# Kernel tuning notes

Hardware: AMD Instinct MI355X
Metric: run time of the kernel (lower is better)

The kernel has to match this reference:

```python
import jax, jax.numpy as jnp
import numpy as np

DN = ('NCHW', 'OIHW', 'NCHW')


def conv2d(x, w, b, stride):
    y = jax.lax.conv_general_dilated(x, w, (stride, stride), 'VALID', dimension_numbers=DN)
    return y + b[None, :, None, None]


def split_heads(t, heads):
    # 'B (c h) H W -> B h (H W) c'  (channel index = c*heads + h)
    B, C, H, W = t.shape
    c = C // heads
    t = t.reshape(B, c, heads, H * W)
    return jnp.transpose(t, (0, 2, 3, 1))  # [B, h, HW, c]


def setup_inputs() -> dict:
    key = jax.random.key(0)
    ks = jax.random.split(key, 7)
    B, dim, H, W = 4, 256, 128, 128
    inner, p = 256, 8
    s = 0.02
    return {
        'x':  jax.random.normal(ks[0], (B, dim, H, W), jnp.float32),
        'Wq': jax.random.normal(ks[1], (inner, dim, 1, 1), jnp.float32) * s,
        'bq': jax.random.normal(ks[2], (inner,), jnp.float32) * s,
        'Wk': jax.random.normal(ks[3], (inner, dim, p, p), jnp.float32) * s,
        'bk': jax.random.normal(ks[4], (inner,), jnp.float32) * s,
        'Wv': jax.random.normal(ks[5], (inner, dim, p, p), jnp.float32) * s,
        'bv': jax.random.normal(ks[6], (inner,), jnp.float32) * s,
    }


def reference(x, Wq, bq, Wk, bk, Wv, bv):
    heads = 8
    p = Wk.shape[-1]
    B, C, H, W = x.shape
    q = conv2d(x, Wq, bq, 1)      # [B, inner, H, W]
    k = conv2d(x, Wk, bk, p)      # [B, inner, H/p, W/p]
    v = conv2d(x, Wv, bv, p)
    q = split_heads(q, heads)     # [B, h, HW, c]
    k = split_heads(k, heads)     # [B, h, K, c]
    v = split_heads(v, heads)
    # NOTE: original module applies no 1/sqrt(d) scaling
    dots = jnp.einsum('bhnc,bhkc->bhnk', q, k)
    attn = jax.nn.softmax(dots, axis=-1)
    out = jnp.einsum('bhnk,bhkc->bhnc', attn, v)  # [B, h, HW, c]
    # 'B h (H W) c -> B (c h) H W'
    c = out.shape[-1]
    out = jnp.transpose(out, (0, 3, 1, 2)).reshape(B, c * heads, H, W)
    return out
```

## Files before the change

### kernel.cpp

```cpp
#include <hip/hip_runtime.h>
#include <stdint.h>

typedef short sh4 __attribute__((ext_vector_type(4)));
typedef short short8 __attribute__((ext_vector_type(8)));
typedef float f32x4 __attribute__((ext_vector_type(4)));
typedef _Float16 half4 __attribute__((ext_vector_type(4)));
typedef _Float16 half8 __attribute__((ext_vector_type(8)));
typedef unsigned int uint2v __attribute__((ext_vector_type(2)));

__device__ __forceinline__ short f2h(float f) {
    _Float16 h = (_Float16)f;
    return __builtin_bit_cast(short, h);
}

__device__ __forceinline__ f32x4 mfma_k32(short8 a, short8 b, f32x4 c) {
    return __builtin_amdgcn_mfma_f32_16x16x32_f16(
        __builtin_bit_cast(half8, a), __builtin_bit_cast(half8, b), c, 0, 0, 0);
}
__device__ __forceinline__ f32x4 mfma_k16(half4 a, half4 b, f32x4 c) {
    return __builtin_amdgcn_mfma_f32_16x16x16f16(a, b, c, 0, 0, 0);
}
__device__ __forceinline__ unsigned int pkrtz(float a, float b) {
    return __builtin_bit_cast(unsigned int, __builtin_amdgcn_cvt_pkrtz(a, b));
}


__device__ __forceinline__ void transpose64(const float* __restrict__ src,
                                            short* __restrict__ dst,
                                            int srcSlowStride, int dstRowStride) {
    __shared__ float tile[64][65];
    const int t = threadIdx.x;
#pragma unroll
    for (int i = 0; i < 16; ++i) {
        int idx = i * 256 + t;
        int fast = idx & 63, slow = idx >> 6;
        tile[slow][fast] = src[(long)slow * srcSlowStride + fast];
    }
    __syncthreads();
#pragma unroll
    for (int i = 0; i < 2; ++i) {
        int ch = i * 256 + t;
        int fast = ch >> 3, sg = ch & 7;
        short8 v;
#pragma unroll
        for (int j = 0; j < 8; ++j) v[j] = f2h(tile[sg * 8 + j][fast]);
        *(short8*)(dst + (long)fast * dstRowStride + sg * 8) = v;
    }
}

__global__ __launch_bounds__(256) void k_pack_x(const float* __restrict__ x,
                                                short* __restrict__ xn) {
    int bi = blockIdx.x;
    int ct = bi & 3, pxt = (bi >> 2) & 255, b = bi >> 10;
    const float* src = x + (((long)(b * 256 + ct * 64)) << 14) + (long)pxt * 64;
    short* dst = xn + (((long)(b << 14) + pxt * 64) * 256) + ct * 64;
    transpose64(src, dst, 16384, 256);
}

__global__ __launch_bounds__(256) void k_pack_w(const float* __restrict__ wk,
                                                const float* __restrict__ wv,
                                                short* __restrict__ wp) {
    int bi = blockIdx.x;
    int ct = bi & 3, oc = bi >> 2;
    const float* base = (oc < 256) ? (wk + (long)oc * 16384) : (wv + (long)(oc - 256) * 16384);
    const float* src = base + ct * 4096;
    short* dst = wp + (long)oc * 16384 + ct * 64;
    transpose64(src, dst, 64, 256);
}

__global__ __launch_bounds__(256) void k_pack_wq(const float* __restrict__ wq,
                                                 short* __restrict__ wqp) {
    int i = blockIdx.x * 256 + threadIdx.x;
    wqp[i] = f2h(wq[i]);
}

__global__ __launch_bounds__(256) void k_kv_gemm(const short* __restrict__ xn,
                                                 const short* __restrict__ wp,
                                                 float* __restrict__ part) {
    __shared__ short Al[128 * 64];
    __shared__ short Bl[64 * 64];
    int bid = blockIdx.x;
    int wg = (bid & 7) * 64 + (bid >> 3);
    int nb = wg & 7, pm = (wg >> 3) & 7, kc = wg >> 6;
    int t = threadIdx.x, l = t & 63, w = t >> 6;
    int wm = w >> 1, wn = w & 1;
    int low = l & 15, q = l >> 4;

    f32x4 acc[4][2];
#pragma unroll
    for (int mt = 0; mt < 4; ++mt)
#pragma unroll
        for (int nt = 0; nt < 2; ++nt) acc[mt][nt] = (f32x4){0.f, 0.f, 0.f, 0.f};

    for (int kk = 0; kk < 32; ++kk) {
        short8 va[4], vb[2];
#pragma unroll
        for (int i = 0; i < 4; ++i) {
            int g = i * 256 + t;
            int row = g >> 3, lg = g & 7;
            int patch = pm * 128 + row;
            int kg = kc * 2048 + kk * 64 + lg * 8;
            int dydx = kg >> 8, cc = kg & 255;
            int bb = patch >> 8, pid = patch & 255;
            int ph = pid >> 4, pw = pid & 15;
            int px = (ph * 8 + (dydx >> 3)) * 128 + pw * 8 + (dydx & 7);
            va[i] = *(const short8*)(xn + ((long)(bb << 14) + px) * 256 + cc);
        }
#pragma unroll
        for (int i = 0; i < 2; ++i) {
            int g = i * 256 + t;
            int row = g >> 3, lg = g & 7;
            int oc = nb * 64 + row;
            int kg = kc * 2048 + kk * 64 + lg * 8;
            vb[i] = *(const short8*)(wp + (long)oc * 16384 + kg);
        }
#pragma unroll
        for (int i = 0; i < 4; ++i) {
            int g = i * 256 + t;
            int row = g >> 3, lg = g & 7;
            *(short8*)(Al + row * 64 + ((lg ^ (row & 7)) * 8)) = va[i];
        }
#pragma unroll
        for (int i = 0; i < 2; ++i) {
            int g = i * 256 + t;
            int row = g >> 3, lg = g & 7;
            *(short8*)(Bl + row * 64 + ((lg ^ (row & 7)) * 8)) = vb[i];
        }
        __syncthreads();
#pragma unroll
        for (int ks = 0; ks < 2; ++ks) {
            short8 af[4], bf[2];
#pragma unroll
            for (int mt = 0; mt < 4; ++mt) {
                int row = wm * 64 + mt * 16 + low;
                int lg = ks * 4 + q;
                af[mt] = *(const short8*)(Al + row * 64 + ((lg ^ (row & 7)) * 8));
            }
#pragma unroll
            for (int nt = 0; nt < 2; ++nt) {
                int row = wn * 32 + nt * 16 + low;
                int lg = ks * 4 + q;
                bf[nt] = *(const short8*)(Bl + row * 64 + ((lg ^ (row & 7)) * 8));
            }
#pragma unroll
            for (int mt = 0; mt < 4; ++mt)
#pragma unroll
                for (int nt = 0; nt < 2; ++nt)
                    acc[mt][nt] = mfma_k32(af[mt], bf[nt], acc[mt][nt]);
        }
        __syncthreads();
    }
#pragma unroll
    for (int mt = 0; mt < 4; ++mt) {
        int patch = pm * 128 + wm * 64 + mt * 16 + q * 4;
#pragma unroll
        for (int nt = 0; nt < 2; ++nt) {
            int oc = nb * 64 + wn * 32 + nt * 16 + low;
#pragma unroll
            for (int r = 0; r < 4; ++r)
                part[((long)kc * 1024 + patch + r) * 512 + oc] = acc[mt][nt][r];
        }
    }
}

__global__ __launch_bounds__(256) void k_kv_fin(const float* __restrict__ part,
                                                const float* __restrict__ bk,
                                                const float* __restrict__ bv,
                                                short* __restrict__ kp,
                                                short* __restrict__ vp) {
    int idx = blockIdx.x * 256 + threadIdx.x;
    int oc = idx & 511, patch = idx >> 9;
    float s = 0.f;
#pragma unroll
    for (int kc = 0; kc < 8; ++kc) s += part[(long)kc * 524288 + idx];
    int b = patch >> 8, key = patch & 255;
    if (oc < 256) {
        s += bk[oc];
        kp[(((long)(b * 8 + (oc & 7)) * 256) + key) * 32 + (oc >> 3)] = f2h(s);
    } else {
        int o = oc - 256;
        s += bv[o];
        vp[(((long)(b * 8 + (o & 7)) * 32) + (o >> 3)) * 256 + key] = f2h(s);
    }
}

__global__ __launch_bounds__(256) void k_q_gemm(const short* __restrict__ xn,
                                                const short* __restrict__ wqp,
                                                const float* __restrict__ bq,
                                                short* __restrict__ qp) {
    __shared__ short Tb[64 * 256];
    int bi = blockIdx.x;
    int b = bi >> 8, tile = bi & 255;
    long px0 = (long)tile * 64;
    int t = threadIdx.x, l = t & 63, w = t >> 6;
    int low = l & 15, q = l >> 4;

    const short* xb = xn + (((long)(b << 14)) + px0) * 256;

    float bqv[4];
#pragma unroll
    for (int nt = 0; nt < 4; ++nt) bqv[nt] = bq[w * 64 + nt * 16 + low];

    f32x4 acc[4][4];
#pragma unroll
    for (int mt = 0; mt < 4; ++mt)
#pragma unroll
        for (int nt = 0; nt < 4; ++nt) acc[mt][nt] = (f32x4){0.f, 0.f, 0.f, 0.f};

#pragma unroll
    for (int kstep = 0; kstep < 8; ++kstep) {
        short8 af[4], bf[4];
#pragma unroll
        for (int mt = 0; mt < 4; ++mt)
            af[mt] = *(const short8*)(xb + (mt * 16 + low) * 256 + kstep * 32 + q * 8);
#pragma unroll
        for (int nt = 0; nt < 4; ++nt)
            bf[nt] = *(const short8*)(wqp + (w * 64 + nt * 16 + low) * 256 + kstep * 32 + q * 8);
#pragma unroll
        for (int mt = 0; mt < 4; ++mt)
#pragma unroll
            for (int nt = 0; nt < 4; ++nt)
                acc[mt][nt] = mfma_k32(af[mt], bf[nt], acc[mt][nt]);
    }
#pragma unroll
    for (int mt = 0; mt < 4; ++mt)
#pragma unroll
        for (int nt = 0; nt < 4; ++nt) {
            int oc = w * 64 + nt * 16 + low;
            int h8 = oc & 7, cc = oc >> 3;
            int gi = h8 * 4 + (cc >> 3);
#pragma unroll
            for (int r = 0; r < 4; ++r) {
                int px = mt * 16 + q * 4 + r;
                Tb[px * 256 + ((gi ^ (px & 7)) * 8) + (cc & 7)] =
                    f2h(acc[mt][nt][r] + bqv[nt]);
            }
        }
    __syncthreads();
#pragma unroll
    for (int i = 0; i < 8; ++i) {
        int g = i * 256 + t;
        int pxl = g >> 5, g16 = g & 31;
        int hh = g16 >> 2, oct = g16 & 3;
        short8 v = *(const short8*)(Tb + pxl * 256 + ((g16 ^ (pxl & 7)) * 8));
        *(short8*)(qp + (((long)(b * 8 + hh) * 16384) + px0 + pxl) * 32 + oct * 8) = v;
    }
}

__global__ __launch_bounds__(256) void k_attn(const short* __restrict__ qp,
                                              const short* __restrict__ kp,
                                              const short* __restrict__ vp,
                                              float* __restrict__ out) {
    __shared__ short Kl[256 * 32];
    __shared__ short Vl[32 * 264];
    int bi = blockIdx.x;
    int tile = bi & 127, h = (bi >> 7) & 7, b = bi >> 10;
    int bh = b * 8 + h;
    long px0 = (long)tile * 128;
    int t = threadIdx.x, l = t & 63, w = t >> 6;
    int low = l & 15, q = l >> 4;

    const short* kbase = kp + (long)bh * 8192;
    const short* vbase = vp + (long)bh * 8192;
    const short* qbase = qp + (long)bh * 16384 * 32;

#pragma unroll
    for (int i = 0; i < 4; ++i) {
        int g = i * 256 + t;
        *(short8*)(Kl + g * 8) = *(const short8*)(kbase + g * 8);
    }
#pragma unroll
    for (int i = 0; i < 4; ++i) {
        int g = i * 256 + t;
        int c = g >> 5, k8 = g & 31;
        *(short8*)(Vl + c * 264 + k8 * 8) = *(const short8*)(vbase + c * 256 + k8 * 8);
    }
    short8 bq2[2];
#pragma unroll
    for (int nt = 0; nt < 2; ++nt) {
        long px = px0 + w * 32 + nt * 16 + low;
        bq2[nt] = *(const short8*)(qbase + px * 32 + q * 8);
    }
    __syncthreads();

#pragma unroll 1
    for (int nt = 0; nt < 2; ++nt) {
        float m = -1e30f;
#pragma unroll
        for (int mt = 0; mt < 16; ++mt) {
            short8 ak = *(const short8*)(Kl + (mt * 16 + low) * 32 + q * 8);
            f32x4 d = mfma_k32(ak, bq2[nt], (f32x4){0.f, 0.f, 0.f, 0.f});
            m = fmaxf(m, fmaxf(fmaxf(d[0], d[1]), fmaxf(d[2], d[3])));
        }
        m = fmaxf(m, __shfl_xor(m, 16));
        m = fmaxf(m, __shfl_xor(m, 32));

        float s = 0.f;
        uint2v pk[16];
#pragma unroll
        for (int mt = 0; mt < 16; ++mt) {
            short8 ak = *(const short8*)(Kl + (mt * 16 + low) * 32 + q * 8);
            f32x4 d = mfma_k32(ak, bq2[nt], (f32x4){0.f, 0.f, 0.f, 0.f});
            float p0 = __expf(d[0] - m);
            float p1 = __expf(d[1] - m);
            float p2 = __expf(d[2] - m);
            float p3 = __expf(d[3] - m);
            s += (p0 + p1) + (p2 + p3);
            pk[mt][0] = pkrtz(p0, p1);
            pk[mt][1] = pkrtz(p2, p3);
        }
        s += __shfl_xor(s, 16);
        s += __shfl_xor(s, 32);
        float inv = 1.0f / s;

        f32x4 o2[2];
        o2[0] = (f32x4){0.f, 0.f, 0.f, 0.f};
        o2[1] = (f32x4){0.f, 0.f, 0.f, 0.f};
#pragma unroll
        for (int kc = 0; kc < 16; ++kc) {
            half4 pb = __builtin_bit_cast(half4, pk[kc]);
#pragma unroll
            for (int ct = 0; ct < 2; ++ct) {
                half4 av = __builtin_bit_cast(half4,
                    *(const sh4*)(Vl + (ct * 16 + low) * 264 + kc * 16 + q * 4));
                o2[ct] = mfma_k16(av, pb, o2[ct]);
            }
        }
        long px = px0 + w * 32 + nt * 16 + low;
#pragma unroll
        for (int ct = 0; ct < 2; ++ct)
#pragma unroll
            for (int r = 0; r < 4; ++r) {
                int c = ct * 16 + q * 4 + r;
                out[(((long)(b * 256 + c * 8 + h)) << 14) + px] = o2[ct][r] * inv;
            }
    }
}

extern "C" void kernel_launch(void* const* d_in, const int* in_sizes, int n_in,
                              void* d_out, int out_size, void* d_ws, size_t ws_size,
                              hipStream_t stream) {
    const float* x  = (const float*)d_in[0];
    const float* Wq = (const float*)d_in[1];
    const float* bq = (const float*)d_in[2];
    const float* Wk = (const float*)d_in[3];
    const float* bk = (const float*)d_in[4];
    const float* Wv = (const float*)d_in[5];
    const float* bv = (const float*)d_in[6];
    float* out = (float*)d_out;

    char* ws = (char*)d_ws;
    const size_t OFF_XN = 0;
    const size_t OFF_Q  = 33554432;
    const size_t OFF_WP = 67108864;
    const size_t OFF_WQ = 83886080;
    const size_t OFF_KP = 84017152;
    const size_t OFF_VP = 84541440;
    const size_t OFF_PT = 85065728;
    const size_t NEEDED = 118620160;
    if (ws_size < NEEDED) return;

    short* xn  = (short*)(ws + OFF_XN);
    short* qp  = (short*)(ws + OFF_Q);
    short* wp  = (short*)(ws + OFF_WP);
    short* wqp = (short*)(ws + OFF_WQ);
    short* kp  = (short*)(ws + OFF_KP);
    short* vp  = (short*)(ws + OFF_VP);
    float* part= (float*)(ws + OFF_PT);

    k_pack_x <<<dim3(4096), dim3(256), 0, stream>>>(x, xn);
    k_pack_w <<<dim3(2048), dim3(256), 0, stream>>>(Wk, Wv, wp);
    k_pack_wq<<<dim3(256),  dim3(256), 0, stream>>>(Wq, wqp);
    k_kv_gemm<<<dim3(512),  dim3(256), 0, stream>>>(xn, wp, part);
    k_kv_fin <<<dim3(2048), dim3(256), 0, stream>>>(part, bk, bv, kp, vp);
    k_q_gemm <<<dim3(1024), dim3(256), 0, stream>>>(xn, wqp, bq, qp);
    k_attn   <<<dim3(4096), dim3(256), 0, stream>>>(qp, kp, vp, out);
}
```

Baseline: 169.8 us.

## Process two query tiles per wave in attention and halve grid

Each attention block now covers 256 pixels, so the grid is halved. Each wave handles two 16-pixel query tiles at once, which lets every K and V LDS read feed two MFMAs and gives the scheduler independent work to interleave. The per-block K/V staging into LDS is amortized over twice as many queries. The PV MFMA loop is wrapped in s_setprio. Register pressure roughly doubles for the probability packs and accumulators, which may cut occupancy.

```diff
diff --git a/kernel.cpp b/kernel.cpp
--- a/kernel.cpp
+++ b/kernel.cpp
@@ -254,9 +254,9 @@
     __shared__ short Kl[256 * 32];
     __shared__ short Vl[32 * 264];
     int bi = blockIdx.x;
-    int tile = bi & 127, h = (bi >> 7) & 7, b = bi >> 10;
+    int tile = bi & 63, h = (bi >> 6) & 7, b = bi >> 9;
     int bh = b * 8 + h;
-    long px0 = (long)tile * 128;
+    long px0 = (long)tile * 256;
     int t = threadIdx.x, l = t & 63, w = t >> 6;
     int low = l & 15, q = l >> 4;
 
@@ -275,64 +275,80 @@
         int c = g >> 5, k8 = g & 31;
         *(short8*)(Vl + c * 264 + k8 * 8) = *(const short8*)(vbase + c * 256 + k8 * 8);
     }
-    short8 bq2[2];
-#pragma unroll
-    for (int nt = 0; nt < 2; ++nt) {
-        long px = px0 + w * 32 + nt * 16 + low;
-        bq2[nt] = *(const short8*)(qbase + px * 32 + q * 8);
-    }
     __syncthreads();
 
 #pragma unroll 1
-    for (int nt = 0; nt < 2; ++nt) {
-        float m = -1e30f;
+    for (int tt = 0; tt < 2; ++tt) {
+        long pxb = px0 + tt * 128 + w * 32 + low;
+        short8 bq0 = *(const short8*)(qbase + pxb * 32 + q * 8);
+        short8 bq1 = *(const short8*)(qbase + (pxb + 16) * 32 + q * 8);
+
+        float m0 = -1e30f, m1 = -1e30f;
 #pragma unroll
         for (int mt = 0; mt < 16; ++mt) {
             short8 ak = *(const short8*)(Kl + (mt * 16 + low) * 32 + q * 8);
-            f32x4 d = mfma_k32(ak, bq2[nt], (f32x4){0.f, 0.f, 0.f, 0.f});
-            m = fmaxf(m, fmaxf(fmaxf(d[0], d[1]), fmaxf(d[2], d[3])));
-        }
-        m = fmaxf(m, __shfl_xor(m, 16));
-        m = fmaxf(m, __shfl_xor(m, 32));
-
-        float s = 0.f;
-        uint2v pk[16];
+            f32x4 d0 = mfma_k32(ak, bq0, (f32x4){0.f, 0.f, 0.f, 0.f});
+            f32x4 d1 = mfma_k32(ak, bq1, (f32x4){0.f, 0.f, 0.f, 0.f});
+            m0 = fmaxf(m0, fmaxf(fmaxf(d0[0], d0[1]), fmaxf(d0[2], d0[3])));
+            m1 = fmaxf(m1, fmaxf(fmaxf(d1[0], d1[1]), fmaxf(d1[2], d1[3])));
+        }
+        m0 = fmaxf(m0, __shfl_xor(m0, 16));
+        m0 = fmaxf(m0, __shfl_xor(m0, 32));
+        m1 = fmaxf(m1, __shfl_xor(m1, 16));
+        m1 = fmaxf(m1, __shfl_xor(m1, 32));
+
+        float s0 = 0.f, s1 = 0.f;
+        uint2v pk0[16], pk1[16];
 #pragma unroll
         for (int mt = 0; mt < 16; ++mt) {
             short8 ak = *(const short8*)(Kl + (mt * 16 + low) * 32 + q * 8);
-            f32x4 d = mfma_k32(ak, bq2[nt], (f32x4){0.f, 0.f, 0.f, 0.f});
-            float p0 = __expf(d[0] - m);
-            float p1 = __expf(d[1] - m);
-            float p2 = __expf(d[2] - m);
-            float p3 = __expf(d[3] - m);
-            s += (p0 + p1) + (p2 + p3);
-            pk[mt][0] = pkrtz(p0, p1);
-            pk[mt][1] = pkrtz(p2, p3);
-        }
-        s += __shfl_xor(s, 16);
-        s += __shfl_xor(s, 32);
-        float inv = 1.0f / s;
-
-        f32x4 o2[2];
-        o2[0] = (f32x4){0.f, 0.f, 0.f, 0.f};
-        o2[1] = (f32x4){0.f, 0.f, 0.f, 0.f};
+            f32x4 d0 = mfma_k32(ak, bq0, (f32x4){0.f, 0.f, 0.f, 0.f});
+            f32x4 d1 = mfma_k32(ak, bq1, (f32x4){0.f, 0.f, 0.f, 0.f});
+            float a0 = __expf(d0[0] - m0), a1 = __expf(d0[1] - m0);
+            float a2 = __expf(d0[2] - m0), a3 = __expf(d0[3] - m0);
+            float b0 = __expf(d1[0] - m1), b1 = __expf(d1[1] - m1);
+            float b2 = __expf(d1[2] - m1), b3 = __expf(d1[3] - m1);
+            s0 += (a0 + a1) + (a2 + a3);
+            s1 += (b0 + b1) + (b2 + b3);
+            pk0[mt][0] = pkrtz(a0, a1);
+            pk0[mt][1] = pkrtz(a2, a3);
+            pk1[mt][0] = pkrtz(b0, b1);
+            pk1[mt][1] = pkrtz(b2, b3);
+        }
+        s0 += __shfl_xor(s0, 16);
+        s0 += __shfl_xor(s0, 32);
+        s1 += __shfl_xor(s1, 16);
+        s1 += __shfl_xor(s1, 32);
+        float inv0 = 1.0f / s0, inv1 = 1.0f / s1;
+
+        f32x4 o0[2], o1[2];
+        o0[0] = (f32x4){0.f, 0.f, 0.f, 0.f};
+        o0[1] = (f32x4){0.f, 0.f, 0.f, 0.f};
+        o1[0] = (f32x4){0.f, 0.f, 0.f, 0.f};
+        o1[1] = (f32x4){0.f, 0.f, 0.f, 0.f};
+        __builtin_amdgcn_s_setprio(1);
 #pragma unroll
         for (int kc = 0; kc < 16; ++kc) {
-            half4 pb = __builtin_bit_cast(half4, pk[kc]);
+            half4 pb0 = __builtin_bit_cast(half4, pk0[kc]);
+            half4 pb1 = __builtin_bit_cast(half4, pk1[kc]);
 #pragma unroll
             for (int ct = 0; ct < 2; ++ct) {
                 half4 av = __builtin_bit_cast(half4,
                     *(const sh4*)(Vl + (ct * 16 + low) * 264 + kc * 16 + q * 4));
-                o2[ct] = mfma_k16(av, pb, o2[ct]);
-            }
-        }
-        long px = px0 + w * 32 + nt * 16 + low;
+                o0[ct] = mfma_k16(av, pb0, o0[ct]);
+                o1[ct] = mfma_k16(av, pb1, o1[ct]);
+            }
+        }
+        __builtin_amdgcn_s_setprio(0);
+
 #pragma unroll
         for (int ct = 0; ct < 2; ++ct)
 #pragma unroll
             for (int r = 0; r < 4; ++r) {
                 int c = ct * 16 + q * 4 + r;
-                out[(((long)(b * 256 + c * 8 + h)) << 14) + px] = o2[ct][r] * inv;
+                long base = ((long)(b * 256 + c * 8 + h)) << 14;
+                out[base + pxb]      = o0[ct][r] * inv0;
+                out[base + pxb + 16] = o1[ct][r] * inv1;
             }
     }
 }
@@ -374,5 +390,5 @@
     k_kv_gemm<<<dim3(512),  dim3(256), 0, stream>>>(xn, wp, part);
     k_kv_fin <<<dim3(2048), dim3(256), 0, stream>>>(part, bk, bv, kp, vp);
     k_q_gemm <<<dim3(1024), dim3(256), 0, stream>>>(xn, wqp, bq, qp);
-    k_attn   <<<dim3(4096), dim3(256), 0, stream>>>(qp, kp, vp, out);
-}
+    k_attn   <<<dim3(2048), dim3(256), 0, stream>>>(qp, kp, vp, out);
+}
```

New measurement: 174.3 us. 1.03x slower.
